# Kernel optimization log

Measured on AMD Instinct MI355X. Metric: run time of the kernel, lower is better.

The kernel has to match this reference:

```python
import jax, jax.numpy as jnp
import numpy as np

N_GRAPHS = 128   # number of graphs in the batch
G = 128          # nodes per graph (equal-sized ragged blocks for the reference)
D = 512          # node embedding dim (feature_dim)
EPS = 1e-7


def setup_inputs() -> dict:
    key = jax.random.key(0)
    embeddings = jax.random.normal(key, (N_GRAPHS * G, D), dtype=jnp.float32)
    # Precompute block-diagonal strict-upper-triangular mask as gather indices.
    # Equivalent to torch.block_diag(*[triu(ones(g,g), diagonal=1) for g in sizes]).bool()
    iu_r, iu_c = np.triu_indices(G, k=1)                 # per-block triu(.,1) indices
    offsets = (np.arange(N_GRAPHS) * G)[:, None]         # block offsets into [N, N]
    row_idx = jnp.asarray((offsets + iu_r[None, :]).ravel(), dtype=jnp.int32)
    col_idx = jnp.asarray((offsets + iu_c[None, :]).ravel(), dtype=jnp.int32)
    return {"embeddings": embeddings, "row_idx": row_idx, "col_idx": col_idx}


def reference(embeddings, row_idx, col_idx):
    # Full NxN dot-product similarity (N = total nodes across all graphs).
    sims = embeddings @ embeddings.T                     # [N, N]
    m = sims.min()
    M = sims.max()
    sims = (sims - m) / (M - m + EPS)                    # global min-max normalization
    # Gather block-diagonal strict-upper-triangular entries -> flat vector.
    return sims[row_idx, col_idx]                        # [sum_g g*(g-1)/2]
```

## Files before the change

### kernel.cpp

```cpp
#include <hip/hip_runtime.h>
#include <hip/hip_bf16.h>
#include <stdint.h>


typedef __attribute__((ext_vector_type(8))) __bf16 bf16x8;
typedef __attribute__((ext_vector_type(16))) float floatx16;
typedef __attribute__((ext_vector_type(4))) int intx4;
typedef __attribute__((ext_vector_type(16))) int intx16;

#define AS1 __attribute__((address_space(1)))
#define AS3 __attribute__((address_space(3)))

static constexpr int DIM      = 512;
static constexpr int NTILE    = 128;
static constexpr int GX       = 72;
static constexpr int NPAIRIDX = 65 * 128;
static constexpr float QS     = 19.5f;
static constexpr int MARGIN_I = 3042;


static __device__ __forceinline__ unsigned short f2bf_rne(float f) {
  unsigned int u = __float_as_uint(f);
  u += 0x7fffu + ((u >> 16) & 1u);
  return (unsigned short)(u >> 16);
}
static __device__ __forceinline__ int fkey(float f) {
  int s = __float_as_int(f);
  return s >= 0 ? s : (s ^ 0x7fffffff);
}
static __device__ __forceinline__ float funkey(int k) {
  return __int_as_float(k >= 0 ? k : (k ^ 0x7fffffff));
}
static __device__ __forceinline__ int swzd(int row, int c16) {
  return c16 ^ (row & 15);
}
static __device__ __forceinline__ int swz8(int row, int c8) {
  return c8 ^ (row & 7);
}
static __device__ __forceinline__ int qswap(int v) {
  return (v & 0x7A) | ((v & 1) << 2) | ((v >> 2) & 1);
}
static __device__ __forceinline__ int sfun(int row) {
  return (row & 3) ^ ((row >> 3) & 3);
}

__global__ void k_convert(const float* __restrict__ in,
                          unsigned short* __restrict__ bf,
                          char* __restrict__ q,
                          int* __restrict__ ctrl, int n4) {
  int i = blockIdx.x * blockDim.x + threadIdx.x;
  if (i == 0) {
    ctrl[0] = 0x7fffffff; ctrl[1] = (int)0x80000000;
    ctrl[2] = 0x7fffffff;
  }
  if (i >= n4) return;
  float4 v = ((const float4*)in)[i];
  ushort4 o;
  o.x = f2bf_rne(v.x); o.y = f2bf_rne(v.y);
  o.z = f2bf_rne(v.z); o.w = f2bf_rne(v.w);
  ((ushort4*)bf)[i] = o;
  int qx = __float2int_rn(v.x * QS), qy = __float2int_rn(v.y * QS);
  int qz = __float2int_rn(v.z * QS), qw = __float2int_rn(v.w * QS);
  char4 c;
  c.x = (char)min(127, max(-127, qx));
  c.y = (char)min(127, max(-127, qy));
  c.z = (char)min(127, max(-127, qz));
  c.w = (char)min(127, max(-127, qw));
  ((char4*)q)[i] = c;
}

__global__ __launch_bounds__(256) void k_gemm(
    const char* __restrict__ Eq,
    const unsigned short* __restrict__ E,
    int* __restrict__ ipart,
    float* __restrict__ diagblocks,
    int* __restrict__ ctrl) {
  const int x  = blockIdx.x;
  const int tr = blockIdx.y;
  if (x > 64) return;
  const int pi = tr * 65 + x;

  const int tid = threadIdx.x;
  __shared__ __align__(16) char smem[2][24576];
  __shared__ float2 redbuf[4];
  __shared__ int iredbuf[4];

  const int w = tid >> 6, lane = tid & 63;
  const int wr = w >> 1, wc = w & 1;
  const int l31 = lane & 31;
  const int kg  = lane >> 5;

  if (x < 64) {
    const int tc1 = 2 * x + 1;
    if (tc1 <= tr) {
      if (tid == 0) ipart[pi] = 0x7fffffff;
      return;
    }
    const int tc0 = (2 * x > tr) ? 2 * x : tc1;

    const int rowA  = tr  * 128;
    const int rowB0 = tc0 * 128;
    const int rowB1 = tc1 * 128;

    intx16 acc[2][2][2];
#pragma unroll
    for (int b = 0; b < 2; b++)
#pragma unroll
      for (int i = 0; i < 2; i++)
#pragma unroll
        for (int j = 0; j < 2; j++)
#pragma unroll
          for (int r = 0; r < 16; r++) acc[b][i][j][r] = 0;

#define STAGE6(bb, kt) do {                                                   \
    _Pragma("unroll")                                                         \
    for (int jj_ = 0; jj_ < 2; jj_++) {                                       \
      int p_   = jj_ * 256 + tid;                                             \
      int q_   = p_ >> 2;                                                     \
      int row_ = qswap(q_);                                                   \
      int off_ = (kt) * 64 + (((p_ & 3) ^ sfun(row_)) * 16);                  \
      char* d_ = smem[bb] + p_ * 16;                                          \
      __builtin_amdgcn_global_load_lds(                                       \
          (const AS1 unsigned int*)(Eq + (size_t)(rowA + row_) * DIM + off_), \
          (AS3 unsigned int*)d_, 16, 0, 0);                                   \
      __builtin_amdgcn_global_load_lds(                                       \
          (const AS1 unsigned int*)(Eq + (size_t)(rowB0 + row_) * DIM + off_),\
          (AS3 unsigned int*)(d_ + 8192), 16, 0, 0);                          \
      __builtin_amdgcn_global_load_lds(                                       \
          (const AS1 unsigned int*)(Eq + (size_t)(rowB1 + row_) * DIM + off_),\
          (AS3 unsigned int*)(d_ + 16384), 16, 0, 0);                         \
    }                                                                         \
  } while (0)

    const int ra0 = wr * 64 + l31,  ra1 = wr * 64 + 32 + l31;
    const int rb0 = wc * 64 + l31,  rb1 = wc * 64 + 32 + l31;
    const int pa0 = qswap(ra0) * 64, sa0 = sfun(ra0);
    const int pa1 = qswap(ra1) * 64, sa1 = sfun(ra1);
    const int pb0 = qswap(rb0) * 64, sb0 = sfun(rb0);
    const int pb1 = qswap(rb1) * 64, sb1 = sfun(rb1);

    STAGE6(0, 0);
    __syncthreads();

#pragma unroll
    for (int kt = 0; kt < 8; kt++) {
      if (kt + 1 < 8) STAGE6((kt + 1) & 1, kt + 1);
      const char* cb = smem[kt & 1];
#pragma unroll
      for (int ks = 0; ks < 2; ks++) {
        const int c = ks * 2 + kg;
        intx4 af0 = *(const intx4*)(cb +         pa0 + ((c ^ sa0) << 4));
        intx4 af1 = *(const intx4*)(cb +         pa1 + ((c ^ sa1) << 4));
        intx4 b00 = *(const intx4*)(cb + 8192  + pb0 + ((c ^ sb0) << 4));
        intx4 b01 = *(const intx4*)(cb + 8192  + pb1 + ((c ^ sb1) << 4));
        intx4 b10 = *(const intx4*)(cb + 16384 + pb0 + ((c ^ sb0) << 4));
        intx4 b11 = *(const intx4*)(cb + 16384 + pb1 + ((c ^ sb1) << 4));
        acc[0][0][0] = __builtin_amdgcn_mfma_i32_32x32x32_i8(af0, b00, acc[0][0][0], 0, 0, 0);
        acc[1][0][0] = __builtin_amdgcn_mfma_i32_32x32x32_i8(af0, b10, acc[1][0][0], 0, 0, 0);
        acc[0][0][1] = __builtin_amdgcn_mfma_i32_32x32x32_i8(af0, b01, acc[0][0][1], 0, 0, 0);
        acc[1][0][1] = __builtin_amdgcn_mfma_i32_32x32x32_i8(af0, b11, acc[1][0][1], 0, 0, 0);
        acc[0][1][0] = __builtin_amdgcn_mfma_i32_32x32x32_i8(af1, b00, acc[0][1][0], 0, 0, 0);
        acc[1][1][0] = __builtin_amdgcn_mfma_i32_32x32x32_i8(af1, b10, acc[1][1][0], 0, 0, 0);
        acc[0][1][1] = __builtin_amdgcn_mfma_i32_32x32x32_i8(af1, b01, acc[0][1][1], 0, 0, 0);
        acc[1][1][1] = __builtin_amdgcn_mfma_i32_32x32x32_i8(af1, b11, acc[1][1][1], 0, 0, 0);
      }
      __syncthreads();
    }
#undef STAGE6

    int vmin = 0x7fffffff;
#pragma unroll
    for (int b = 0; b < 2; b++)
#pragma unroll
      for (int ti = 0; ti < 2; ti++)
#pragma unroll
        for (int tj = 0; tj < 2; tj++)
#pragma unroll
          for (int r = 0; r < 16; r++) vmin = min(vmin, acc[b][ti][tj][r]);
#pragma unroll
    for (int m_ = 32; m_ >= 1; m_ >>= 1)
      vmin = min(vmin, __shfl_xor(vmin, m_));
    if (lane == 0) iredbuf[w] = vmin;
    __syncthreads();
    if (tid == 0) {
      int mn = iredbuf[0];
      for (int i = 1; i < 4; i++) mn = min(mn, iredbuf[i]);
      ipart[pi] = mn;
      atomicMin(&ctrl[2], mn);
    }
  } else {
    if (tid == 0) ipart[pi] = 0x7fffffff;
    unsigned short* lA = (unsigned short*)&smem[0][0];
    floatx16 acc[2][2];
#pragma unroll
    for (int i = 0; i < 2; i++)
#pragma unroll
      for (int j = 0; j < 2; j++)
#pragma unroll
        for (int r = 0; r < 16; r++) acc[i][j][r] = 0.f;

    const int rowBase = tr * 128;

    for (int kb = 0; kb < 4; kb++) {
      const int kBase = kb * 128;
#pragma unroll
      for (int j = 0; j < 8; j++) {
        int p   = (w * 8 + j) * 64 + lane;
        int row = p >> 4, c16 = p & 15;
        int sc = swzd(row, c16);
        const unsigned short* gA =
            E + (size_t)(rowBase + row) * DIM + kBase + sc * 8;
        __builtin_amdgcn_global_load_lds((const AS1 unsigned int*)gA,
                                         (AS3 unsigned int*)(lA + p * 8), 16, 0, 0);
      }
      __syncthreads();

#pragma unroll
      for (int ks = 0; ks < 8; ks++) {
        bf16x8 af[2], bfv[2];
        const int c16 = ks * 2 + kg;
#pragma unroll
        for (int t = 0; t < 2; t++) {
          int ra = wr * 64 + t * 32 + l31;
          int rb = wc * 64 + t * 32 + l31;
          af[t]  = *(const bf16x8*)(lA + ra * 128 + swzd(ra, c16) * 8);
          bfv[t] = *(const bf16x8*)(lA + rb * 128 + swzd(rb, c16) * 8);
        }
#pragma unroll
        for (int ti = 0; ti < 2; ti++)
#pragma unroll
          for (int tj = 0; tj < 2; tj++)
            acc[ti][tj] = __builtin_amdgcn_mfma_f32_32x32x16_bf16(
                af[ti], bfv[tj], acc[ti][tj], 0, 0, 0);
      }
      __syncthreads();
    }

    float vmin = 3.4e38f, vmax = -3.4e38f;
#pragma unroll
    for (int ti = 0; ti < 2; ti++)
#pragma unroll
      for (int tj = 0; tj < 2; tj++)
#pragma unroll
        for (int r = 0; r < 16; r++) {
          float v = acc[ti][tj][r];
          vmin = fminf(vmin, v);
          vmax = fmaxf(vmax, v);
        }
#pragma unroll
    for (int m_ = 32; m_ >= 1; m_ >>= 1) {
      vmin = fminf(vmin, __shfl_xor(vmin, m_));
      vmax = fmaxf(vmax, __shfl_xor(vmax, m_));
    }
    if (lane == 0) redbuf[w] = make_float2(vmin, vmax);
    __syncthreads();
    if (tid == 0) {
      float mn = redbuf[0].x, mx = redbuf[0].y;
      for (int i = 1; i < 4; i++) {
        mn = fminf(mn, redbuf[i].x);
        mx = fmaxf(mx, redbuf[i].y);
      }
      atomicMin(&ctrl[0], fkey(mn));
      atomicMax(&ctrl[1], fkey(mx));
    }

    float* Bout = diagblocks + (size_t)tr * (128 * 128);
#pragma unroll
    for (int ti = 0; ti < 2; ti++) {
#pragma unroll
      for (int tj = 0; tj < 2; tj++) {
        int cbase = wc * 64 + tj * 32 + l31;
#pragma unroll
        for (int r = 0; r < 16; r++) {
          int row = wr * 64 + ti * 32 + (r & 3) + 8 * (r >> 2) + 4 * kg;
          Bout[row * 128 + cbase] = acc[ti][tj][r];
        }
      }
    }
  }
}

__global__ __launch_bounds__(256) void k_refine(
    const unsigned short* __restrict__ E,
    const int* __restrict__ ipart, int* __restrict__ ctrl) {
  const int pi = blockIdx.x;
  if (ipart[pi] > ctrl[2] + MARGIN_I) return;
  const int tr = pi / 65, x = pi % 65;
  if (x == 64) return;

  const int tid = threadIdx.x;
  __shared__ __align__(16) unsigned short lA[128 * 64];
  __shared__ __align__(16) unsigned short lB[128 * 64];
  __shared__ float redbuf[4];

  const int w = tid >> 6, lane = tid & 63;
  const int wr = w >> 1, wc = w & 1;
  const int l31 = lane & 31;
  const int kg  = lane >> 5;

  for (int s = 0; s < 2; s++) {
    const int tc = 2 * x + s;
    if (tc <= tr) continue;

    floatx16 acc[2][2];
#pragma unroll
    for (int i = 0; i < 2; i++)
#pragma unroll
      for (int j = 0; j < 2; j++)
#pragma unroll
        for (int r = 0; r < 16; r++) acc[i][j][r] = 0.f;

    const int rowBaseA = tr * 128;
    const int rowBaseB = tc * 128;

    for (int kb = 0; kb < 8; kb++) {
      const int kBase = kb * 64;
#pragma unroll
      for (int j = 0; j < 4; j++) {
        int cb  = (w * 4 + j) * 64;
        int p   = cb + lane;
        int row = p >> 3, c8 = p & 7;
        int sc8 = swz8(row, c8);
        const unsigned short* gA = E + (size_t)(rowBaseA + row) * DIM + kBase + sc8 * 8;
        const unsigned short* gB = E + (size_t)(rowBaseB + row) * DIM + kBase + sc8 * 8;
        __builtin_amdgcn_global_load_lds((const AS1 unsigned int*)gA,
                                         (AS3 unsigned int*)(lA + cb * 8), 16, 0, 0);
        __builtin_amdgcn_global_load_lds((const AS1 unsigned int*)gB,
                                         (AS3 unsigned int*)(lB + cb * 8), 16, 0, 0);
      }
      __syncthreads();

#pragma unroll
      for (int ks = 0; ks < 4; ks++) {
        bf16x8 af[2], bfv[2];
        const int c8 = ks * 2 + kg;
#pragma unroll
        for (int t = 0; t < 2; t++) {
          int ra = wr * 64 + t * 32 + l31;
          int rb = wc * 64 + t * 32 + l31;
          af[t]  = *(const bf16x8*)(lA + (ra * 8 + swz8(ra, c8)) * 8);
          bfv[t] = *(const bf16x8*)(lB + (rb * 8 + swz8(rb, c8)) * 8);
        }
#pragma unroll
        for (int ti = 0; ti < 2; ti++)
#pragma unroll
          for (int tj = 0; tj < 2; tj++)
            acc[ti][tj] = __builtin_amdgcn_mfma_f32_32x32x16_bf16(
                af[ti], bfv[tj], acc[ti][tj], 0, 0, 0);
      }
      __syncthreads();
    }

    float vmin = 3.4e38f;
#pragma unroll
    for (int ti = 0; ti < 2; ti++)
#pragma unroll
      for (int tj = 0; tj < 2; tj++)
#pragma unroll
        for (int r = 0; r < 16; r++) vmin = fminf(vmin, acc[ti][tj][r]);
#pragma unroll
    for (int m_ = 32; m_ >= 1; m_ >>= 1)
      vmin = fminf(vmin, __shfl_xor(vmin, m_));
    if (lane == 0) redbuf[w] = vmin;
    __syncthreads();
    if (tid == 0) {
      float mn = redbuf[0];
      for (int i = 1; i < 4; i++) mn = fminf(mn, redbuf[i]);
      atomicMin(&ctrl[0], fkey(mn));
    }
    __syncthreads();
  }
}

__global__ __launch_bounds__(256) void k_gather(
    const int* __restrict__ rix, const int* __restrict__ cix,
    const float* __restrict__ blocks, const int* __restrict__ ctrl,
    float* __restrict__ out, int n) {
  int i = blockIdx.x * blockDim.x + threadIdx.x;
  if (i >= n) return;
  float m   = funkey(ctrl[0]);
  float M   = funkey(ctrl[1]);
  float inv = 1.0f / (M - m + 1e-7f);
  int r = rix[i], c = cix[i];
  int g = r >> 7;
  float v = blocks[((size_t)g << 14) + ((r & 127) << 7) + (c & 127)];
  out[i] = (v - m) * inv;
}

extern "C" void kernel_launch(void* const* d_in, const int* in_sizes, int n_in,
                              void* d_out, int out_size, void* d_ws, size_t ws_size,
                              hipStream_t stream) {
  const float* emb = (const float*)d_in[0];
  const int* rix   = (const int*)d_in[1];
  const int* cix   = (const int*)d_in[2];

  char* ws = (char*)d_ws;
  int* ctrl           = (int*)ws;
  unsigned short* Ebf = (unsigned short*)(ws + 256);
  char* Eq            = (char*)(ws + 256 + (16u << 20));
  float* diagblocks   = (float*)(ws + 256 + (24u << 20));
  int* ipart          = (int*)(ws + 256 + (32u << 20));

  int n4 = in_sizes[0] / 4;

  k_convert<<<(n4 + 255) / 256, 256, 0, stream>>>(emb, Ebf, Eq, ctrl, n4);

  k_gemm<<<dim3(GX, 128), 256, 0, stream>>>(Eq, Ebf, ipart, diagblocks, ctrl);

  k_refine<<<NPAIRIDX, 256, 0, stream>>>(Ebf, ipart, ctrl);

  k_gather<<<(out_size + 255) / 256, 256, 0, stream>>>(rix, cix, diagblocks,
                                                       ctrl, (float*)d_out,
                                                       out_size);
}
```

Baseline: 193.7 us.

## Balance triangular tile pairs with a wraparound mapping, one B tile per block

Each GEMM block of the int8 similarity pass now handles one 128x128 tile pair chosen by a cyclic (tr, tr+1+x mod 128) mapping. Before, each block handled one A tile against two B tiles and roughly half the blocks exited at once. The refine kernel uses the same mapping, and the GEMM's LDS staging shrinks to two operand tiles with a launch-bounds occupancy hint of 4. The aim is to spread the upper-triangle work evenly across the grid and raise occupancy. In exchange, A-tile reuse per block is lost, and 64 tile pairs are computed twice, which is harmless for the min reduction.

```diff
diff --git a/kernel.cpp b/kernel.cpp
--- a/kernel.cpp
+++ b/kernel.cpp
@@ -69,7 +69,7 @@
   ((char4*)q)[i] = c;
 }
 
-__global__ __launch_bounds__(256) void k_gemm(
+__global__ __launch_bounds__(256, 4) void k_gemm(
     const char* __restrict__ Eq,
     const unsigned short* __restrict__ E,
     int* __restrict__ ipart,
@@ -81,7 +81,7 @@
   const int pi = tr * 65 + x;
 
   const int tid = threadIdx.x;
-  __shared__ __align__(16) char smem[2][24576];
+  __shared__ __align__(16) char smem[2][16384];
   __shared__ float2 redbuf[4];
   __shared__ int iredbuf[4];
 
@@ -91,28 +91,20 @@
   const int kg  = lane >> 5;
 
   if (x < 64) {
-    const int tc1 = 2 * x + 1;
-    if (tc1 <= tr) {
-      if (tid == 0) ipart[pi] = 0x7fffffff;
-      return;
-    }
-    const int tc0 = (2 * x > tr) ? 2 * x : tc1;
-
-    const int rowA  = tr  * 128;
-    const int rowB0 = tc0 * 128;
-    const int rowB1 = tc1 * 128;
-
-    intx16 acc[2][2][2];
-#pragma unroll
-    for (int b = 0; b < 2; b++)
-#pragma unroll
-      for (int i = 0; i < 2; i++)
-#pragma unroll
-        for (int j = 0; j < 2; j++)
-#pragma unroll
-          for (int r = 0; r < 16; r++) acc[b][i][j][r] = 0;
-
-#define STAGE6(bb, kt) do {                                                   \
+    const int tcw = (tr + 1 + x) & 127;
+    const int a = min(tr, tcw), b = max(tr, tcw);
+    const int rowA = a * 128;
+    const int rowB = b * 128;
+
+    intx16 acc[2][2];
+#pragma unroll
+    for (int i = 0; i < 2; i++)
+#pragma unroll
+      for (int j = 0; j < 2; j++)
+#pragma unroll
+        for (int r = 0; r < 16; r++) acc[i][j][r] = 0;
+
+#define STAGE4(bb, kt) do {                                                   \
     _Pragma("unroll")                                                         \
     for (int jj_ = 0; jj_ < 2; jj_++) {                                       \
       int p_   = jj_ * 256 + tid;                                             \
@@ -124,11 +116,8 @@
           (const AS1 unsigned int*)(Eq + (size_t)(rowA + row_) * DIM + off_), \
           (AS3 unsigned int*)d_, 16, 0, 0);                                   \
       __builtin_amdgcn_global_load_lds(                                       \
-          (const AS1 unsigned int*)(Eq + (size_t)(rowB0 + row_) * DIM + off_),\
+          (const AS1 unsigned int*)(Eq + (size_t)(rowB + row_) * DIM + off_), \
           (AS3 unsigned int*)(d_ + 8192), 16, 0, 0);                          \
-      __builtin_amdgcn_global_load_lds(                                       \
-          (const AS1 unsigned int*)(Eq + (size_t)(rowB1 + row_) * DIM + off_),\
-          (AS3 unsigned int*)(d_ + 16384), 16, 0, 0);                         \
     }                                                                         \
   } while (0)
 
@@ -139,44 +128,36 @@
     const int pb0 = qswap(rb0) * 64, sb0 = sfun(rb0);
     const int pb1 = qswap(rb1) * 64, sb1 = sfun(rb1);
 
-    STAGE6(0, 0);
+    STAGE4(0, 0);
     __syncthreads();
 
 #pragma unroll
     for (int kt = 0; kt < 8; kt++) {
-      if (kt + 1 < 8) STAGE6((kt + 1) & 1, kt + 1);
+      if (kt + 1 < 8) STAGE4((kt + 1) & 1, kt + 1);
       const char* cb = smem[kt & 1];
 #pragma unroll
       for (int ks = 0; ks < 2; ks++) {
         const int c = ks * 2 + kg;
-        intx4 af0 = *(const intx4*)(cb +         pa0 + ((c ^ sa0) << 4));
-        intx4 af1 = *(const intx4*)(cb +         pa1 + ((c ^ sa1) << 4));
-        intx4 b00 = *(const intx4*)(cb + 8192  + pb0 + ((c ^ sb0) << 4));
-        intx4 b01 = *(const intx4*)(cb + 8192  + pb1 + ((c ^ sb1) << 4));
-        intx4 b10 = *(const intx4*)(cb + 16384 + pb0 + ((c ^ sb0) << 4));
-        intx4 b11 = *(const intx4*)(cb + 16384 + pb1 + ((c ^ sb1) << 4));
-        acc[0][0][0] = __builtin_amdgcn_mfma_i32_32x32x32_i8(af0, b00, acc[0][0][0], 0, 0, 0);
-        acc[1][0][0] = __builtin_amdgcn_mfma_i32_32x32x32_i8(af0, b10, acc[1][0][0], 0, 0, 0);
-        acc[0][0][1] = __builtin_amdgcn_mfma_i32_32x32x32_i8(af0, b01, acc[0][0][1], 0, 0, 0);
-        acc[1][0][1] = __builtin_amdgcn_mfma_i32_32x32x32_i8(af0, b11, acc[1][0][1], 0, 0, 0);
-        acc[0][1][0] = __builtin_amdgcn_mfma_i32_32x32x32_i8(af1, b00, acc[0][1][0], 0, 0, 0);
-        acc[1][1][0] = __builtin_amdgcn_mfma_i32_32x32x32_i8(af1, b10, acc[1][1][0], 0, 0, 0);
-        acc[0][1][1] = __builtin_amdgcn_mfma_i32_32x32x32_i8(af1, b01, acc[0][1][1], 0, 0, 0);
-        acc[1][1][1] = __builtin_amdgcn_mfma_i32_32x32x32_i8(af1, b11, acc[1][1][1], 0, 0, 0);
+        intx4 af0 = *(const intx4*)(cb +        pa0 + ((c ^ sa0) << 4));
+        intx4 af1 = *(const intx4*)(cb +        pa1 + ((c ^ sa1) << 4));
+        intx4 bf0 = *(const intx4*)(cb + 8192 + pb0 + ((c ^ sb0) << 4));
+        intx4 bf1 = *(const intx4*)(cb + 8192 + pb1 + ((c ^ sb1) << 4));
+        acc[0][0] = __builtin_amdgcn_mfma_i32_32x32x32_i8(af0, bf0, acc[0][0], 0, 0, 0);
+        acc[0][1] = __builtin_amdgcn_mfma_i32_32x32x32_i8(af0, bf1, acc[0][1], 0, 0, 0);
+        acc[1][0] = __builtin_amdgcn_mfma_i32_32x32x32_i8(af1, bf0, acc[1][0], 0, 0, 0);
+        acc[1][1] = __builtin_amdgcn_mfma_i32_32x32x32_i8(af1, bf1, acc[1][1], 0, 0, 0);
       }
       __syncthreads();
     }
-#undef STAGE6
+#undef STAGE4
 
     int vmin = 0x7fffffff;
 #pragma unroll
-    for (int b = 0; b < 2; b++)
-#pragma unroll
-      for (int ti = 0; ti < 2; ti++)
-#pragma unroll
-        for (int tj = 0; tj < 2; tj++)
-#pragma unroll
-          for (int r = 0; r < 16; r++) vmin = min(vmin, acc[b][ti][tj][r]);
+    for (int ti = 0; ti < 2; ti++)
+#pragma unroll
+      for (int tj = 0; tj < 2; tj++)
+#pragma unroll
+        for (int r = 0; r < 16; r++) vmin = min(vmin, acc[ti][tj][r]);
 #pragma unroll
     for (int m_ = 32; m_ >= 1; m_ >>= 1)
       vmin = min(vmin, __shfl_xor(vmin, m_));
@@ -287,6 +268,8 @@
   if (ipart[pi] > ctrl[2] + MARGIN_I) return;
   const int tr = pi / 65, x = pi % 65;
   if (x == 64) return;
+  const int tcw = (tr + 1 + x) & 127;
+  const int a = min(tr, tcw), b = max(tr, tcw);
 
   const int tid = threadIdx.x;
   __shared__ __align__(16) unsigned short lA[128 * 64];
@@ -298,77 +281,71 @@
   const int l31 = lane & 31;
   const int kg  = lane >> 5;
 
-  for (int s = 0; s < 2; s++) {
-    const int tc = 2 * x + s;
-    if (tc <= tr) continue;
-
-    floatx16 acc[2][2];
-#pragma unroll
-    for (int i = 0; i < 2; i++)
-#pragma unroll
-      for (int j = 0; j < 2; j++)
-#pragma unroll
-        for (int r = 0; r < 16; r++) acc[i][j][r] = 0.f;
-
-    const int rowBaseA = tr * 128;
-    const int rowBaseB = tc * 128;
-
-    for (int kb = 0; kb < 8; kb++) {
-      const int kBase = kb * 64;
-#pragma unroll
-      for (int j = 0; j < 4; j++) {
-        int cb  = (w * 4 + j) * 64;
-        int p   = cb + lane;
-        int row = p >> 3, c8 = p & 7;
-        int sc8 = swz8(row, c8);
-        const unsigned short* gA = E + (size_t)(rowBaseA + row) * DIM + kBase + sc8 * 8;
-        const unsigned short* gB = E + (size_t)(rowBaseB + row) * DIM + kBase + sc8 * 8;
-        __builtin_amdgcn_global_load_lds((const AS1 unsigned int*)gA,
-                                         (AS3 unsigned int*)(lA + cb * 8), 16, 0, 0);
-        __builtin_amdgcn_global_load_lds((const AS1 unsigned int*)gB,
-                                         (AS3 unsigned int*)(lB + cb * 8), 16, 0, 0);
-      }
-      __syncthreads();
-
-#pragma unroll
-      for (int ks = 0; ks < 4; ks++) {
-        bf16x8 af[2], bfv[2];
-        const int c8 = ks * 2 + kg;
-#pragma unroll
-        for (int t = 0; t < 2; t++) {
-          int ra = wr * 64 + t * 32 + l31;
-          int rb = wc * 64 + t * 32 + l31;
-          af[t]  = *(const bf16x8*)(lA + (ra * 8 + swz8(ra, c8)) * 8);
-          bfv[t] = *(const bf16x8*)(lB + (rb * 8 + swz8(rb, c8)) * 8);
-        }
-#pragma unroll
-        for (int ti = 0; ti < 2; ti++)
-#pragma unroll
-          for (int tj = 0; tj < 2; tj++)
-            acc[ti][tj] = __builtin_amdgcn_mfma_f32_32x32x16_bf16(
-                af[ti], bfv[tj], acc[ti][tj], 0, 0, 0);
-      }
-      __syncthreads();
-    }
-
-    float vmin = 3.4e38f;
-#pragma unroll
-    for (int ti = 0; ti < 2; ti++)
-#pragma unroll
-      for (int tj = 0; tj < 2; tj++)
-#pragma unroll
-        for (int r = 0; r < 16; r++) vmin = fminf(vmin, acc[ti][tj][r]);
-#pragma unroll
-    for (int m_ = 32; m_ >= 1; m_ >>= 1)
-      vmin = fminf(vmin, __shfl_xor(vmin, m_));
-    if (lane == 0) redbuf[w] = vmin;
-    __syncthreads();
-    if (tid == 0) {
-      float mn = redbuf[0];
-      for (int i = 1; i < 4; i++) mn = fminf(mn, redbuf[i]);
-      atomicMin(&ctrl[0], fkey(mn));
-    }
-    __syncthreads();
+  floatx16 acc[2][2];
+#pragma unroll
+  for (int i = 0; i < 2; i++)
+#pragma unroll
+    for (int j = 0; j < 2; j++)
+#pragma unroll
+      for (int r = 0; r < 16; r++) acc[i][j][r] = 0.f;
+
+  const int rowBaseA = a * 128;
+  const int rowBaseB = b * 128;
+
+  for (int kb = 0; kb < 8; kb++) {
+    const int kBase = kb * 64;
+#pragma unroll
+    for (int j = 0; j < 4; j++) {
+      int cb  = (w * 4 + j) * 64;
+      int p   = cb + lane;
+      int row = p >> 3, c8 = p & 7;
+      int sc8 = swz8(row, c8);
+      const unsigned short* gA = E + (size_t)(rowBaseA + row) * DIM + kBase + sc8 * 8;
+      const unsigned short* gB = E + (size_t)(rowBaseB + row) * DIM + kBase + sc8 * 8;
+      __builtin_amdgcn_global_load_lds((const AS1 unsigned int*)gA,
+                                       (AS3 unsigned int*)(lA + cb * 8), 16, 0, 0);
+      __builtin_amdgcn_global_load_lds((const AS1 unsigned int*)gB,
+                                       (AS3 unsigned int*)(lB + cb * 8), 16, 0, 0);
+    }
+    __syncthreads();
+
+#pragma unroll
+    for (int ks = 0; ks < 4; ks++) {
+      bf16x8 af[2], bfv[2];
+      const int c8 = ks * 2 + kg;
+#pragma unroll
+      for (int t = 0; t < 2; t++) {
+        int ra = wr * 64 + t * 32 + l31;
+        int rb = wc * 64 + t * 32 + l31;
+        af[t]  = *(const bf16x8*)(lA + (ra * 8 + swz8(ra, c8)) * 8);
+        bfv[t] = *(const bf16x8*)(lB + (rb * 8 + swz8(rb, c8)) * 8);
+      }
+#pragma unroll
+      for (int ti = 0; ti < 2; ti++)
+#pragma unroll
+        for (int tj = 0; tj < 2; tj++)
+          acc[ti][tj] = __builtin_amdgcn_mfma_f32_32x32x16_bf16(
+              af[ti], bfv[tj], acc[ti][tj], 0, 0, 0);
+    }
+    __syncthreads();
+  }
+
+  float vmin = 3.4e38f;
+#pragma unroll
+  for (int ti = 0; ti < 2; ti++)
+#pragma unroll
+    for (int tj = 0; tj < 2; tj++)
+#pragma unroll
+      for (int r = 0; r < 16; r++) vmin = fminf(vmin, acc[ti][tj][r]);
+#pragma unroll
+  for (int m_ = 32; m_ >= 1; m_ >>= 1)
+    vmin = fminf(vmin, __shfl_xor(vmin, m_));
+  if (lane == 0) redbuf[w] = vmin;
+  __syncthreads();
+  if (tid == 0) {
+    float mn = redbuf[0];
+    for (int i = 1; i < 4; i++) mn = fminf(mn, redbuf[i]);
+    atomicMin(&ctrl[0], fkey(mn));
   }
 }
 
```

New measurement: 219.6 us. +13.4%, slower.
